# Performance work log

Hardware: AMD Instinct MI355X
Metric: run time of the kernel (lower is better)

The kernel has to match this reference:

```python
import jax, jax.numpy as jnp
import numpy as np

EPS = 1e-5

def _layernorm(x, gamma, beta):
    mu = jnp.mean(x, axis=-1, keepdims=True)
    var = jnp.mean(jnp.square(x - mu), axis=-1, keepdims=True)
    return (x - mu) * jax.lax.rsqrt(var + EPS) * gamma + beta

def setup_inputs() -> dict:
    key = jax.random.key(0)
    kx, kw = jax.random.split(key)
    N, D, BIT = 65536, 1024, 64
    X = jax.random.normal(kx, (N, D), dtype=jnp.float32)
    # xavier_uniform with gain=0.5 for weight [BIT, D]
    limit = 0.5 * np.sqrt(6.0 / (D + BIT))
    W = jax.random.uniform(kw, (BIT, D), minval=-limit, maxval=limit, dtype=jnp.float32)
    b = jnp.zeros((BIT,), dtype=jnp.float32)
    ln1_g = jnp.ones((D,), dtype=jnp.float32)
    ln1_b = jnp.zeros((D,), dtype=jnp.float32)
    ln2_g = jnp.ones((BIT,), dtype=jnp.float32)
    ln2_b = jnp.zeros((BIT,), dtype=jnp.float32)
    return {"X": X, "W": W, "b": b, "ln1_g": ln1_g, "ln1_b": ln1_b, "ln2_g": ln2_g, "ln2_b": ln2_b}

def reference(X, W, b, ln1_g, ln1_b, ln2_g, ln2_b):
    # LayerNorm -> Linear -> LayerNorm
    xn = _layernorm(X, ln1_g, ln1_b)                       # [N, D]
    logits = jnp.einsum('nd,bd->nb', xn, W) + b            # [N, BIT]
    logits = _layernorm(logits, ln2_g, ln2_b)
    # mean-center over batch, tanh, sign-binarize
    logits = logits - jnp.mean(logits, axis=0, keepdims=True)
    H = jnp.tanh(0.5 * logits)
    B = jnp.where(H >= 0.0, jnp.int8(1), jnp.int8(-1))
    return H, B
```

## Files before the change

### kernel.cpp

```cpp
#include <hip/hip_runtime.h>
#include <stdint.h>

#define N_ROWS 65536
#define D_IN   1024
#define NBIT   64
#define LN_EPS 1e-5f

typedef __attribute__((ext_vector_type(8))) _Float16 f16x8;
typedef __attribute__((ext_vector_type(4))) float f32x4;

__device__ __forceinline__ void gload_lds16(const void* g, void* l) {
    __builtin_amdgcn_global_load_lds(
        (const __attribute__((address_space(1))) uint32_t*)g,
        (__attribute__((address_space(3))) uint32_t*)l, 16, 0, 0);
}

__global__ void prep_kernel(const float* __restrict__ W, const float* __restrict__ bias,
                            const float* __restrict__ g1, const float* __restrict__ b1,
                            _Float16* __restrict__ whi, _Float16* __restrict__ wlo,
                            float* __restrict__ u, float* __restrict__ v) {
    int bit = blockIdx.x;
    int t   = threadIdx.x;
    int nt  = bit >> 4, bl = bit & 15;
    float su = 0.f, sv = 0.f;
    for (int d = t; d < D_IN; d += 256) {
        float w  = W[bit * D_IN + d];
        float gw = w * g1[d];
        su += gw;
        sv += w * b1[d];
        int kt = d >> 5, gg = (d >> 3) & 3, j = d & 7;
        size_t idx = (((size_t)(kt * 4 + nt)) * 64 + gg * 16 + bl) * 8 + j;
        _Float16 h = (_Float16)gw;
        whi[idx] = h;
        wlo[idx] = (_Float16)((gw - (float)h) * 2048.0f);
    }
    __shared__ float s1[256], s2[256];
    s1[t] = su; s2[t] = sv;
    __syncthreads();
    for (int off = 128; off > 0; off >>= 1) {
        if (t < off) { s1[t] += s1[t + off]; s2[t] += s2[t + off]; }
        __syncthreads();
    }
    if (t == 0) { u[bit] = s1[0]; v[bit] = s2[0] + bias[bit]; }
}

__global__ void __launch_bounds__(256) main_kernel(
        const float* __restrict__ X,
        const _Float16* __restrict__ whi, const _Float16* __restrict__ wlo,
        const float* __restrict__ u, const float* __restrict__ v,
        const float* __restrict__ g2, const float* __restrict__ b2,
        float* __restrict__ L, float* __restrict__ P) {
    __shared__ _Float16 lw[2][8192];
    int tid  = threadIdx.x;
    int wid  = tid >> 6, lane = tid & 63;
    int g    = lane >> 4, r16 = lane & 15;
    int row_base = blockIdx.x * 64 + wid * 16;

    const float* xrow = X + (size_t)(row_base + r16) * D_IN + g * 8;

    const _Float16* gbase = ((wid & 2) ? wlo : whi) + (wid & 1) * 2048 + lane * 8;
    const int lofs = ((wid & 2) ? 4096 : 0) + (wid & 1) * 2048;

#pragma unroll
    for (int r = 0; r < 4; ++r)
        gload_lds16(gbase + r * 512, &lw[0][lofs + r * 512]);

    f32x4 acc_h0[4], acc_h1[4], acc_m[4], acc_ll[4];
#pragma unroll
    for (int nt = 0; nt < 4; ++nt) {
        acc_h0[nt] = (f32x4){0.f, 0.f, 0.f, 0.f};
        acc_h1[nt] = (f32x4){0.f, 0.f, 0.f, 0.f};
        acc_m[nt]  = (f32x4){0.f, 0.f, 0.f, 0.f};
        acc_ll[nt] = (f32x4){0.f, 0.f, 0.f, 0.f};
    }
    float sum = 0.f, sumsq = 0.f;

    __syncthreads();

    for (int c = 0; c < 16; ++c) {
        const _Float16* lwb = &lw[c & 1][0];
        if (c + 1 < 16) {
            const _Float16* gs = gbase + (c + 1) * 4096;
            _Float16* ld = &lw[(c + 1) & 1][lofs];
#pragma unroll
            for (int r = 0; r < 4; ++r)
                gload_lds16(gs + r * 512, ld + r * 512);
        }
#pragma unroll
        for (int t2 = 0; t2 < 2; ++t2) {
            int t = c * 2 + t2;
            float4 x0 = *(const float4*)(xrow + t * 32);
            float4 x1 = *(const float4*)(xrow + t * 32 + 4);
            float xs[8] = {x0.x, x0.y, x0.z, x0.w, x1.x, x1.y, x1.z, x1.w};
            f16x8 ahi, alo;
            float ts = 0.f, tq = 0.f;
#pragma unroll
            for (int j = 0; j < 8; ++j) {
                ts += xs[j];
                tq = fmaf(xs[j], xs[j], tq);
                _Float16 h = (_Float16)xs[j];
                ahi[j] = h;
                alo[j] = (_Float16)((xs[j] - (float)h) * 2048.0f);
            }
            sum += ts;
            sumsq += tq;
            const _Float16* bhp = lwb + t2 * 2048 + lane * 8;
#pragma unroll
            for (int nt = 0; nt < 4; ++nt) {
                f16x8 bh = *(const f16x8*)(bhp + nt * 512);
                f16x8 bl = *(const f16x8*)(bhp + 4096 + nt * 512);
                if (t2 == 0)
                    acc_h0[nt] = __builtin_amdgcn_mfma_f32_16x16x32_f16(ahi, bh, acc_h0[nt], 0, 0, 0);
                else
                    acc_h1[nt] = __builtin_amdgcn_mfma_f32_16x16x32_f16(ahi, bh, acc_h1[nt], 0, 0, 0);
                acc_m[nt]  = __builtin_amdgcn_mfma_f32_16x16x32_f16(ahi, bl, acc_m[nt], 0, 0, 0);
                acc_m[nt]  = __builtin_amdgcn_mfma_f32_16x16x32_f16(alo, bh, acc_m[nt], 0, 0, 0);
                acc_ll[nt] = __builtin_amdgcn_mfma_f32_16x16x32_f16(alo, bl, acc_ll[nt], 0, 0, 0);
            }
        }
        __syncthreads();
    }

    sum   += __shfl_xor(sum, 16);   sum   += __shfl_xor(sum, 32);
    sumsq += __shfl_xor(sumsq, 16); sumsq += __shfl_xor(sumsq, 32);
    float mu   = sum * (1.f / 1024.f);
    float var  = sumsq * (1.f / 1024.f) - mu * mu;
    float rstd = rsqrtf(var + LN_EPS);

    float uv[4], vv[4], g2v[4], b2v[4];
#pragma unroll
    for (int nt = 0; nt < 4; ++nt) {
        int bitc = nt * 16 + r16;
        uv[nt] = u[bitc]; vv[nt] = v[bitc]; g2v[nt] = g2[bitc]; b2v[nt] = b2[bitc];
    }
    float mu_m[4], rs_m[4];
#pragma unroll
    for (int reg = 0; reg < 4; ++reg) {
        int m = g * 4 + reg;
        mu_m[reg] = __shfl(mu, m);
        rs_m[reg] = __shfl(rstd, m);
    }

    float lg[4][4];
#pragma unroll
    for (int nt = 0; nt < 4; ++nt)
#pragma unroll
        for (int reg = 0; reg < 4; ++reg) {
            float dot = (acc_h0[nt][reg] + acc_h1[nt][reg])
                      + acc_m[nt][reg] * (1.0f / 2048.0f)
                      + acc_ll[nt][reg] * (1.0f / 4194304.0f);
            lg[nt][reg] = rs_m[reg] * dot - rs_m[reg] * mu_m[reg] * uv[nt] + vv[nt];
        }

#pragma unroll
    for (int reg = 0; reg < 4; ++reg) {
        float s1 = lg[0][reg] + lg[1][reg] + lg[2][reg] + lg[3][reg];
        float s2 = lg[0][reg]*lg[0][reg] + lg[1][reg]*lg[1][reg]
                 + lg[2][reg]*lg[2][reg] + lg[3][reg]*lg[3][reg];
#pragma unroll
        for (int m = 1; m <= 8; m <<= 1) {
            s1 += __shfl_xor(s1, m);
            s2 += __shfl_xor(s2, m);
        }
        float mean = s1 * (1.f / 64.f);
        float va   = s2 * (1.f / 64.f) - mean * mean;
        float rs2  = rsqrtf(va + LN_EPS);
#pragma unroll
        for (int nt = 0; nt < 4; ++nt)
            lg[nt][reg] = (lg[nt][reg] - mean) * rs2 * g2v[nt] + b2v[nt];
    }

#pragma unroll
    for (int reg = 0; reg < 4; ++reg) {
        size_t row = (size_t)(row_base + g * 4 + reg);
#pragma unroll
        for (int nt = 0; nt < 4; ++nt)
            L[row * 64 + nt * 16 + r16] = lg[nt][reg];
    }

#pragma unroll
    for (int nt = 0; nt < 4; ++nt) {
        float cs = lg[nt][0] + lg[nt][1] + lg[nt][2] + lg[nt][3];
        cs += __shfl_xor(cs, 16);
        cs += __shfl_xor(cs, 32);
        if (g == 0)
            P[((size_t)blockIdx.x * 4 + wid) * 64 + nt * 16 + r16] = cs;
    }
}

__global__ void reduce_kernel(const float* __restrict__ P, float* __restrict__ cm) {
    int bit = blockIdx.x, t = threadIdx.x;
    float s = 0.f;
    for (int p = t; p < 4096; p += 256) s += P[(size_t)p * 64 + bit];
    __shared__ float sh[256];
    sh[t] = s;
    __syncthreads();
    for (int off = 128; off > 0; off >>= 1) {
        if (t < off) sh[t] += sh[t + off];
        __syncthreads();
    }
    if (t == 0) cm[bit] = sh[0] * (1.f / (float)N_ROWS);
}

__global__ void final_kernel(const float* __restrict__ L, const float* __restrict__ cm,
                             float* __restrict__ out) {
    __shared__ float cms[64];
    if (threadIdx.x < 64) cms[threadIdx.x] = cm[threadIdx.x];
    __syncthreads();
    const float4* L4 = (const float4*)L;
    float4* H4 = (float4*)out;
    float4* B4 = (float4*)(out + (size_t)N_ROWS * NBIT);
    int total = N_ROWS * NBIT / 4;
    for (int i = blockIdx.x * blockDim.x + threadIdx.x; i < total;
         i += gridDim.x * blockDim.x) {
        float4 x = L4[i];
        int bb = (i & 15) * 4;
        float4 h, bo;
        h.x = tanhf(0.5f * (x.x - cms[bb + 0]));
        h.y = tanhf(0.5f * (x.y - cms[bb + 1]));
        h.z = tanhf(0.5f * (x.z - cms[bb + 2]));
        h.w = tanhf(0.5f * (x.w - cms[bb + 3]));
        bo.x = h.x >= 0.f ? 1.f : -1.f;
        bo.y = h.y >= 0.f ? 1.f : -1.f;
        bo.z = h.z >= 0.f ? 1.f : -1.f;
        bo.w = h.w >= 0.f ? 1.f : -1.f;
        H4[i] = h;
        B4[i] = bo;
    }
}

extern "C" void kernel_launch(void* const* d_in, const int* in_sizes, int n_in,
                              void* d_out, int out_size, void* d_ws, size_t ws_size,
                              hipStream_t stream) {
    (void)in_sizes; (void)n_in; (void)out_size; (void)ws_size;
    const float* X  = (const float*)d_in[0];
    const float* W  = (const float*)d_in[1];
    const float* bb = (const float*)d_in[2];
    const float* g1 = (const float*)d_in[3];
    const float* b1 = (const float*)d_in[4];
    const float* g2 = (const float*)d_in[5];
    const float* b2 = (const float*)d_in[6];

    char* ws = (char*)d_ws;
    _Float16* whi = (_Float16*)ws;
    _Float16* wlo = (_Float16*)(ws + 131072);
    float* u  = (float*)(ws + 262144);
    float* v  = (float*)(ws + 266240);
    float* P  = (float*)(ws + 270336);
    float* cm = (float*)(ws + 270336 + 4096 * 64 * 4);

    float* out = (float*)d_out;
    float* L   = out + (size_t)N_ROWS * NBIT;

    prep_kernel<<<64, 256, 0, stream>>>(W, bb, g1, b1, whi, wlo, u, v);
    main_kernel<<<1024, 256, 0, stream>>>(X, whi, wlo, u, v, g2, b2, L, P);
    reduce_kernel<<<64, 256, 0, stream>>>(P, cm);
    final_kernel<<<2048, 256, 0, stream>>>(L, cm, out);
}
```

Baseline: 97.62 us.

## Software-pipeline X loads with explicit double-buffer unroll and transpose partial sums

The main loop is unrolled by two with explicit ping-pong buffers, so X rows for the next chunk are prefetched into registers together with the LDS weight staging, hiding global load latency behind the MFMA work. The partial column-sum buffer P is transposed to bit-major order so the reduce kernel reads contiguous memory instead of strided columns. The cost is higher register pressure from the eight float4 prefetch registers, which may lower occupancy.

```diff
diff --git a/kernel.cpp b/kernel.cpp
--- a/kernel.cpp
+++ b/kernel.cpp
@@ -13,6 +13,35 @@
     __builtin_amdgcn_global_load_lds(
         (const __attribute__((address_space(1))) uint32_t*)g,
         (__attribute__((address_space(3))) uint32_t*)l, 16, 0, 0);
+}
+
+__device__ __forceinline__ f32x4 mfma16(f16x8 a, f16x8 b, f32x4 c) {
+    return __builtin_amdgcn_mfma_f32_16x16x32_f16(a, b, c, 0, 0, 0);
+}
+
+__device__ __forceinline__ void do_tstep(float4 x0, float4 x1,
+        const _Float16* bhp, f32x4* acc_h, f32x4* acc_m, f32x4* acc_ll,
+        float& sum, float& sumsq) {
+    float xs[8] = {x0.x, x0.y, x0.z, x0.w, x1.x, x1.y, x1.z, x1.w};
+    f16x8 ahi, alo;
+#pragma unroll
+    for (int j = 0; j < 8; ++j) {
+        float xv = xs[j];
+        sum += xv;
+        sumsq = fmaf(xv, xv, sumsq);
+        _Float16 h = (_Float16)xv;
+        ahi[j] = h;
+        alo[j] = (_Float16)((xv - (float)h) * 2048.0f);
+    }
+#pragma unroll
+    for (int nt = 0; nt < 4; ++nt) {
+        f16x8 bh = *(const f16x8*)(bhp + nt * 512);
+        f16x8 bl = *(const f16x8*)(bhp + 4096 + nt * 512);
+        acc_h[nt]  = mfma16(ahi, bh, acc_h[nt]);
+        acc_m[nt]  = mfma16(ahi, bl, acc_m[nt]);
+        acc_m[nt]  = mfma16(alo, bh, acc_m[nt]);
+        acc_ll[nt] = mfma16(alo, bl, acc_ll[nt]);
+    }
 }
 
 __global__ void prep_kernel(const float* __restrict__ W, const float* __restrict__ bias,
@@ -61,9 +90,22 @@
     const _Float16* gbase = ((wid & 2) ? wlo : whi) + (wid & 1) * 2048 + lane * 8;
     const int lofs = ((wid & 2) ? 4096 : 0) + (wid & 1) * 2048;
 
-#pragma unroll
-    for (int r = 0; r < 4; ++r)
-        gload_lds16(gbase + r * 512, &lw[0][lofs + r * 512]);
+#define STAGEW(cc, buf) do {                                         \
+        const _Float16* gs_ = gbase + (cc) * 4096;                   \
+        _Float16* ld_ = &lw[buf][lofs];                              \
+        gload_lds16(gs_,         ld_);                               \
+        gload_lds16(gs_ + 512,   ld_ + 512);                         \
+        gload_lds16(gs_ + 1024,  ld_ + 1024);                        \
+        gload_lds16(gs_ + 1536,  ld_ + 1536);                        \
+    } while (0)
+
+#define PREFX(cc, r0, r1, r2, r3) do {                               \
+        const float* xp_ = xrow + (cc) * 64;                         \
+        r0 = *(const float4*)(xp_);                                  \
+        r1 = *(const float4*)(xp_ + 4);                              \
+        r2 = *(const float4*)(xp_ + 32);                             \
+        r3 = *(const float4*)(xp_ + 36);                             \
+    } while (0)
 
     f32x4 acc_h0[4], acc_h1[4], acc_m[4], acc_ll[4];
 #pragma unroll
@@ -74,49 +116,30 @@
         acc_ll[nt] = (f32x4){0.f, 0.f, 0.f, 0.f};
     }
     float sum = 0.f, sumsq = 0.f;
-
-    __syncthreads();
-
-    for (int c = 0; c < 16; ++c) {
-        const _Float16* lwb = &lw[c & 1][0];
-        if (c + 1 < 16) {
-            const _Float16* gs = gbase + (c + 1) * 4096;
-            _Float16* ld = &lw[(c + 1) & 1][lofs];
-#pragma unroll
-            for (int r = 0; r < 4; ++r)
-                gload_lds16(gs + r * 512, ld + r * 512);
-        }
-#pragma unroll
-        for (int t2 = 0; t2 < 2; ++t2) {
-            int t = c * 2 + t2;
-            float4 x0 = *(const float4*)(xrow + t * 32);
-            float4 x1 = *(const float4*)(xrow + t * 32 + 4);
-            float xs[8] = {x0.x, x0.y, x0.z, x0.w, x1.x, x1.y, x1.z, x1.w};
-            f16x8 ahi, alo;
-            float ts = 0.f, tq = 0.f;
-#pragma unroll
-            for (int j = 0; j < 8; ++j) {
-                ts += xs[j];
-                tq = fmaf(xs[j], xs[j], tq);
-                _Float16 h = (_Float16)xs[j];
-                ahi[j] = h;
-                alo[j] = (_Float16)((xs[j] - (float)h) * 2048.0f);
-            }
-            sum += ts;
-            sumsq += tq;
-            const _Float16* bhp = lwb + t2 * 2048 + lane * 8;
-#pragma unroll
-            for (int nt = 0; nt < 4; ++nt) {
-                f16x8 bh = *(const f16x8*)(bhp + nt * 512);
-                f16x8 bl = *(const f16x8*)(bhp + 4096 + nt * 512);
-                if (t2 == 0)
-                    acc_h0[nt] = __builtin_amdgcn_mfma_f32_16x16x32_f16(ahi, bh, acc_h0[nt], 0, 0, 0);
-                else
-                    acc_h1[nt] = __builtin_amdgcn_mfma_f32_16x16x32_f16(ahi, bh, acc_h1[nt], 0, 0, 0);
-                acc_m[nt]  = __builtin_amdgcn_mfma_f32_16x16x32_f16(ahi, bl, acc_m[nt], 0, 0, 0);
-                acc_m[nt]  = __builtin_amdgcn_mfma_f32_16x16x32_f16(alo, bh, acc_m[nt], 0, 0, 0);
-                acc_ll[nt] = __builtin_amdgcn_mfma_f32_16x16x32_f16(alo, bl, acc_ll[nt], 0, 0, 0);
-            }
+    float4 xa0, xa1, xa2, xa3, xb0, xb1, xb2, xb3;
+
+    PREFX(0, xa0, xa1, xa2, xa3);
+    STAGEW(0, 0);
+    __syncthreads();
+
+    for (int c2 = 0; c2 < 8; ++c2) {
+        int c = 2 * c2;
+        PREFX(c + 1, xb0, xb1, xb2, xb3);
+        STAGEW(c + 1, 1);
+        {
+            const _Float16* bhp = &lw[0][0] + lane * 8;
+            do_tstep(xa0, xa1, bhp,        acc_h0, acc_m, acc_ll, sum, sumsq);
+            do_tstep(xa2, xa3, bhp + 2048, acc_h1, acc_m, acc_ll, sum, sumsq);
+        }
+        __syncthreads();
+        if (c2 < 7) {
+            PREFX(c + 2, xa0, xa1, xa2, xa3);
+            STAGEW(c + 2, 0);
+        }
+        {
+            const _Float16* bhp = &lw[1][0] + lane * 8;
+            do_tstep(xb0, xb1, bhp,        acc_h0, acc_m, acc_ll, sum, sumsq);
+            do_tstep(xb2, xb3, bhp + 2048, acc_h1, acc_m, acc_ll, sum, sumsq);
         }
         __syncthreads();
     }
@@ -184,14 +207,16 @@
         cs += __shfl_xor(cs, 16);
         cs += __shfl_xor(cs, 32);
         if (g == 0)
-            P[((size_t)blockIdx.x * 4 + wid) * 64 + nt * 16 + r16] = cs;
-    }
+            P[(size_t)(nt * 16 + r16) * 4096 + blockIdx.x * 4 + wid] = cs;
+    }
+#undef STAGEW
+#undef PREFX
 }
 
 __global__ void reduce_kernel(const float* __restrict__ P, float* __restrict__ cm) {
     int bit = blockIdx.x, t = threadIdx.x;
     float s = 0.f;
-    for (int p = t; p < 4096; p += 256) s += P[(size_t)p * 64 + bit];
+    for (int p = t; p < 4096; p += 256) s += P[(size_t)bit * 4096 + p];
     __shared__ float sh[256];
     sh[t] = s;
     __syncthreads();
@@ -247,7 +272,7 @@
     float* u  = (float*)(ws + 262144);
     float* v  = (float*)(ws + 266240);
     float* P  = (float*)(ws + 270336);
-    float* cm = (float*)(ws + 270336 + 4096 * 64 * 4);
+    float* cm = (float*)(ws + 270336 + 64 * 4096 * 4);
 
     float* out = (float*)d_out;
     float* L   = out + (size_t)N_ROWS * NBIT;
```

Result: no change. 98.09 us (+0.5%).
